# Kernel tuning notes

Hardware: AMD Instinct MI355X
Metric: run time of the kernel (lower is better)

Reference implementation:

```python
import jax, jax.numpy as jnp
import numpy as np

B, N, C = 4, 4096, 128
IK, CK = 9, 9  # inner_k, cross_k
BN_EPS = 1e-5


def setup_inputs() -> dict:
    key = jax.random.key(0)
    ks = jax.random.split(key, 8)
    d = {}
    d["x"] = jax.random.normal(ks[0], (B, N, C), jnp.float32)
    d["y"] = jax.random.normal(ks[1], (B, N, C), jnp.float32)
    d["x_mask"] = jnp.ones((B, N), jnp.float32)
    d["y_mask"] = jnp.ones((B, N), jnp.float32)
    specs = [("mr0", C, 2 * C), ("mr1", C, 2 * C), ("fc", C, C), ("f1", 4 * C, C), ("f2", C, 4 * C)]
    for (name, o, i), k in zip(specs, jax.random.split(ks[2], len(specs))):
        d[name + "_W"] = jax.random.normal(k, (o, i), jnp.float32) * 0.05
        d[name + "_b"] = jnp.zeros((o,), jnp.float32)
        d[name + "_g"] = jnp.ones((o,), jnp.float32)
        d[name + "_beta"] = jnp.zeros((o,), jnp.float32)
        d[name + "_m"] = jnp.zeros((o,), jnp.float32)
        d[name + "_v"] = jnp.ones((o,), jnp.float32)
    return d


def _sqdist(a, b):
    # a: [B,Na,C], b: [B,Nb,C] -> [B,Na,Nb]
    return (jnp.sum(a * a, -1)[:, :, None] + jnp.sum(b * b, -1)[:, None, :]
            - 2.0 * jnp.einsum('bnc,bmc->bnm', a, b))


def _knn(x, y):
    # neighbor indices into concat([x;y]) for every node: [B, Nx+Ny, IK+CK]
    Nx = x.shape[1]
    i_xx = jax.lax.top_k(-_sqdist(x, x), IK)[1]
    i_xy = jax.lax.top_k(-_sqdist(x, y), CK)[1] + Nx
    i_yy = jax.lax.top_k(-_sqdist(y, y), IK)[1] + Nx
    i_yx = jax.lax.top_k(-_sqdist(y, x), CK)[1]
    return jnp.concatenate([jnp.concatenate([i_xx, i_xy], -1),
                            jnp.concatenate([i_yy, i_yx], -1)], axis=1)


def _bn(h, g, b, m, v):
    # eval-mode BatchNorm over channel (last) axis
    return (h - m) * jax.lax.rsqrt(v + BN_EPS) * g + b


def _gelu(h):
    return jax.nn.gelu(h, approximate=False)


def _mrconv(f, nbr, W, b, g, be, m, v):
    # f: [B,Nt,C], nbr: [B,Nt,K] -> Conv(2C->C)+BN+GELU of interleaved [x, max_j(x_j-x_i)]
    xj = jax.vmap(lambda fb, nb: fb[nb])(f, nbr)          # [B,Nt,K,C] gather
    msg = jnp.max(xj - f[:, :, None, :], axis=2)          # [B,Nt,C]
    Bh, Nt, Ch = f.shape
    h = jnp.stack([f, msg], axis=-1).reshape(Bh, Nt, 2 * Ch)  # channel interleave as in torch reshape
    h = jnp.einsum('bnc,oc->bno', h, W) + b
    return _gelu(_bn(h, g, be, m, v))


def _forward(x, x_mask, y, y_mask,
             mr0_W, mr0_b, mr0_g, mr0_beta, mr0_m, mr0_v,
             mr1_W, mr1_b, mr1_g, mr1_beta, mr1_m, mr1_v,
             fc_W, fc_b, fc_g, fc_beta, fc_m, fc_v,
             f1_W, f1_b, f1_g, f1_beta, f1_m, f1_v,
             f2_W, f2_b, f2_g, f2_beta, f2_m, f2_v):
    Nx = x.shape[1]
    nbr = _knn(x, y)
    xy = jnp.concatenate([x, y], axis=1)
    xy = _mrconv(xy, nbr, mr0_W, mr0_b, mr0_g, mr0_beta, mr0_m, mr0_v) + xy
    xy = _mrconv(xy, nbr, mr1_W, mr1_b, mr1_g, mr1_beta, mr1_m, mr1_v) + xy
    xg, yg = xy[:, :Nx], xy[:, Nx:]

    def fc(h):
        return _bn(jnp.einsum('bnc,oc->bno', h, fc_W) + fc_b, fc_g, fc_beta, fc_m, fc_v)

    xo = fc(xg) + x
    yo = fc(yg) + y

    def ffn(h):
        r = h
        h = _gelu(_bn(jnp.einsum('bnc,oc->bno', h, f1_W) + f1_b, f1_g, f1_beta, f1_m, f1_v))
        h = _gelu(_bn(jnp.einsum('bnc,oc->bno', h, f2_W) + f2_b, f2_g, f2_beta, f2_m, f2_v))
        return h + r

    xo = ffn(xo) * x_mask[:, :, None]
    yo = ffn(yo) * y_mask[:, :, None]
    return xo, yo


def reference(x, x_mask, y, y_mask,
              mr0_W, mr0_b, mr0_g, mr0_beta, mr0_m, mr0_v,
              mr1_W, mr1_b, mr1_g, mr1_beta, mr1_m, mr1_v,
              fc_W, fc_b, fc_g, fc_beta, fc_m, fc_v,
              f1_W, f1_b, f1_g, f1_beta, f1_m, f1_v,
              f2_W, f2_b, f2_g, f2_beta, f2_m, f2_v):
    return _forward(x, x_mask, y, y_mask,
                    mr0_W, mr0_b, mr0_g, mr0_beta, mr0_m, mr0_v,
                    mr1_W, mr1_b, mr1_g, mr1_beta, mr1_m, mr1_v,
                    fc_W, fc_b, fc_g, fc_beta, fc_m, fc_v,
                    f1_W, f1_b, f1_g, f1_beta, f1_m, f1_v,
                    f2_W, f2_b, f2_g, f2_beta, f2_m, f2_v)
```

## Files before the change

### kernel.cpp

```cpp
#include <hip/hip_runtime.h>
#include <hip/hip_bf16.h>
#include <float.h>
#include <math.h>

#define BB 4
#define N1 4096
#define NT 8192
#define CH 128
#define NBRS 18
#define ZSEL 2.35f
#define LCAP 40
#define EQ 4096.0f
#define GQGAP 6
#define GQCOV 3

typedef __attribute__((ext_vector_type(8))) short s16x8;
typedef __attribute__((ext_vector_type(16))) float f32x16;

__device__ inline unsigned short f2bf(float v) {
  unsigned u = __float_as_uint(v);
  unsigned r = (u + 0x7FFFu + ((u >> 16) & 1u)) >> 16;
  return (unsigned short)r;
}

__device__ inline unsigned mapf(float f) {
  unsigned u = __float_as_uint(f);
  return (u & 0x80000000u) ? ~u : (u | 0x80000000u);
}

__global__ __launch_bounds__(256) void transpose_k(const float* __restrict__ in,
                                                   float* __restrict__ out,
                                                   int rows, int cols) {
  int t = blockIdx.x * 256 + threadIdx.x;
  if (t < rows * cols) {
    int r = t / cols, c = t % cols;
    out[c * rows + r] = in[t];
  }
}

__global__ __launch_bounds__(256) void norms_concat_k(const float* __restrict__ x,
                                                      const float* __restrict__ y,
                                                      float* __restrict__ xy,
                                                      float* __restrict__ norms) {
  int w = (blockIdx.x * 256 + threadIdx.x) >> 6;
  int lane = threadIdx.x & 63;
  int b = w >> 13, row = w & 8191;
  const float* src = (row < N1) ? (x + ((size_t)b * N1 + row) * CH)
                                : (y + ((size_t)b * N1 + (row - N1)) * CH);
  float2 v = *(const float2*)(src + lane * 2);
  *(float2*)(xy + (size_t)w * CH + lane * 2) = v;
  float s = v.x * v.x + v.y * v.y;
  for (int off = 32; off > 0; off >>= 1) s += __shfl_down(s, off);
  if (lane == 0) norms[w] = s;
}

__global__ __launch_bounds__(256) void cbt_k(const float* __restrict__ xy,
                                             unsigned short* __restrict__ cbt) {
  int t = blockIdx.x * 256 + threadIdx.x;
  int u = t >> 15, p = t & 32767;
  const float* src = xy + (size_t)p * CH + u * 8;
  unsigned hw[4], lw[4];
#pragma unroll
  for (int j = 0; j < 4; ++j) {
    float v0 = src[2 * j], v1 = src[2 * j + 1];
    unsigned short h0 = f2bf(v0), h1 = f2bf(v1);
    float r0 = v0 - __uint_as_float((unsigned)h0 << 16);
    float r1 = v1 - __uint_as_float((unsigned)h1 << 16);
    unsigned short l0 = f2bf(r0), l1 = f2bf(r1);
    hw[j] = (unsigned)h0 | ((unsigned)h1 << 16);
    lw[j] = (unsigned)l0 | ((unsigned)l1 << 16);
  }
  *(uint4*)&cbt[((size_t)u * 32768 + p) * 8] = make_uint4(hw[0], hw[1], hw[2], hw[3]);
  *(uint4*)&cbt[((size_t)(u + 16) * 32768 + p) * 8] = make_uint4(lw[0], lw[1], lw[2], lw[3]);
}

__global__ __launch_bounds__(256) void knn4_k(const unsigned short* __restrict__ cbt,
                                              const float* __restrict__ norms,
                                              int* __restrict__ nbr,
                                              int* __restrict__ cntg,
                                              unsigned* __restrict__ listA,
                                              unsigned* __restrict__ listB,
                                              unsigned short* __restrict__ fbl) {
  __shared__ unsigned short __align__(16) cst[2][32][32][8];
  __shared__ float cn_s[2][32];
  __shared__ unsigned lst[128][2][LCAP];
  __shared__ unsigned short lcnt[128][2];
  const int tid = threadIdx.x;
  const int qblk = blockIdx.x, z = blockIdx.y;
  const int b = z >> 2, combo = z & 3;
  const int qoff = (combo <= 1) ? 0 : N1;
  const int coff = (combo == 0 || combo == 3) ? 0 : N1;
  const int w = tid >> 6;
  const int cl = tid & 31;
  const int h = (tid >> 5) & 1;
  const int h4 = 4 * h;
  const int ql = w * 32 + cl;
  const int q = qblk * 128 + ql;
  const size_t qp = (size_t)b * NT + qoff + q;
  const size_t cb0 = (size_t)b * NT + coff;

  const s16x8* cv = (const s16x8*)cbt;
  s16x8 bh[8], bl[8];
#pragma unroll
  for (int s = 0; s < 8; ++s) {
    bh[s] = cv[(size_t)(2 * s + h) * 32768 + qp];
    bl[s] = cv[(size_t)(16 + 2 * s + h) * 32768 + qp];
  }

  const float nq = norms[qp];
  const float Tc = 128.f - ZSEL * sqrtf(256.f + 4.f * nq);
  int cnt = 0;

  const int su = tid >> 5, sc = tid & 31;
  const char* p0 = (const char*)&cbt[((size_t)(su) * 32768 + cb0 + sc) * 8];
  const char* p1 = (const char*)&cbt[((size_t)(8 + su) * 32768 + cb0 + sc) * 8];
  const char* p2 = (const char*)&cbt[((size_t)(16 + su) * 32768 + cb0 + sc) * 8];
  const char* p3 = (const char*)&cbt[((size_t)(24 + su) * 32768 + cb0 + sc) * 8];
  const float* pn = norms + cb0 + tid;

  uint4 st[4]; float cnreg = 0.f;
  st[0] = *(const uint4*)p0; p0 += 512;
  st[1] = *(const uint4*)p1; p1 += 512;
  st[2] = *(const uint4*)p2; p2 += 512;
  st[3] = *(const uint4*)p3; p3 += 512;
  if (tid < 32) { cnreg = *pn; pn += 32; }
  *(uint4*)&cst[0][su][sc][0] = st[0];
  *(uint4*)&cst[0][8 + su][sc][0] = st[1];
  *(uint4*)&cst[0][16 + su][sc][0] = st[2];
  *(uint4*)&cst[0][24 + su][sc][0] = st[3];
  if (tid < 32) cn_s[0][tid] = cnreg;
  __syncthreads();

  int buf = 0;
  for (int t = 0; t < 128; ++t) {
    if (t < 127) {
      st[0] = *(const uint4*)p0; p0 += 512;
      st[1] = *(const uint4*)p1; p1 += 512;
      st[2] = *(const uint4*)p2; p2 += 512;
      st[3] = *(const uint4*)p3; p3 += 512;
      if (tid < 32) { cnreg = *pn; pn += 32; }
    }
    f32x16 acc = {0.f,0.f,0.f,0.f,0.f,0.f,0.f,0.f,0.f,0.f,0.f,0.f,0.f,0.f,0.f,0.f};
#pragma unroll
    for (int s = 0; s < 8; ++s) {
      s16x8 a0 = *(const s16x8*)&cst[buf][2 * s + h][cl][0];
      s16x8 a1 = *(const s16x8*)&cst[buf][16 + 2 * s + h][cl][0];
      acc = __builtin_amdgcn_mfma_f32_32x32x16_bf16(a0, bh[s], acc, 0, 0, 0);
      acc = __builtin_amdgcn_mfma_f32_32x32x16_bf16(a0, bl[s], acc, 0, 0, 0);
      acc = __builtin_amdgcn_mfma_f32_32x32x16_bf16(a1, bh[s], acc, 0, 0, 0);
    }
    float4 c0 = *(const float4*)&cn_s[buf][h4];
    float4 c1 = *(const float4*)&cn_s[buf][8 + h4];
    float4 c2 = *(const float4*)&cn_s[buf][16 + h4];
    float4 c3 = *(const float4*)&cn_s[buf][24 + h4];
    const float cw[16] = {c0.x, c0.y, c0.z, c0.w, c1.x, c1.y, c1.z, c1.w,
                          c2.x, c2.y, c2.z, c2.w, c3.x, c3.y, c3.z, c3.w};
    const int ib = t * 32 + h4;
#pragma unroll
    for (int g = 0; g < 4; ++g) {
#pragma unroll
      for (int rr = 0; rr < 4; ++rr) {
        const int r = g * 4 + rr;
        float s = fmaf(-2.0f, acc[r], cw[r]);
        if (s <= Tc) {
          int e = (int)((Tc - s) * EQ);
          e = e > 0xFFFFF ? 0xFFFFF : e;
          unsigned key = ((unsigned)e << 12) | (unsigned)(4095 - (ib + g * 8 + rr));
          if (cnt < LCAP) lst[ql][h][cnt] = key;
          ++cnt;
        }
      }
    }
    if (t < 127) {
      *(uint4*)&cst[buf ^ 1][su][sc][0] = st[0];
      *(uint4*)&cst[buf ^ 1][8 + su][sc][0] = st[1];
      *(uint4*)&cst[buf ^ 1][16 + su][sc][0] = st[2];
      *(uint4*)&cst[buf ^ 1][24 + su][sc][0] = st[3];
      if (tid < 32) cn_s[buf ^ 1][tid] = cnreg;
    }
    __syncthreads();
    buf ^= 1;
  }
  lcnt[ql][h] = (unsigned short)cnt;
  __syncthreads();

  if (tid < 128) {
    const int mq = tid;
    const int gq = z * 4096 + qblk * 128 + mq;
    const int c0 = lcnt[mq][0], c1 = lcnt[mq][1];
    const bool over = (c0 > LCAP) || (c1 > LCAP);
    const int n0 = c0 > LCAP ? LCAP : c0;
    const int n1 = c1 > LCAP ? LCAP : c1;
    const int m = n0 + n1;
    unsigned top[10];
#pragma unroll
    for (int j = 0; j < 10; ++j) top[j] = 0u;
    for (int li = 0; li < 2; ++li) {
      const int n = li ? n1 : n0;
      for (int i = 0; i < n; ++i) {
        unsigned key = lst[mq][li][i];
        if (key > top[9]) {
#pragma unroll
          for (int j = 0; j < 10; ++j) {
            bool sw = key > top[j];
            unsigned tv = top[j];
            top[j] = sw ? key : tv;
            key = sw ? tv : key;
          }
        }
      }
    }
    const unsigned e8 = top[8] >> 12, e9 = top[9] >> 12;
    const bool cov = !over && (m >= 9) && (e8 >= GQCOV);
    const bool ok = cov && (m == 9 || (e8 - e9) >= GQGAP);
    const int qg = qblk * 128 + mq;
    const int row = (combo <= 1) ? qg : (N1 + qg);
    const int slot = (combo == 0 || combo == 2) ? 0 : 9;
    const int ioff = (combo == 1 || combo == 2) ? N1 : 0;
    int* dst = nbr + ((size_t)b * NT + row) * NBRS + slot;
    if (ok) {
#pragma unroll
      for (int s = 0; s < 9; ++s)
        dst[s] = (int)(4095u - (top[s] & 0xFFFu)) + ioff;
    } else if (!cov || m > 64) {
      int idx = atomicAdd(&cntg[1], 1);
      listB[idx] = (unsigned)gq;
    } else {
      int idx = atomicAdd(&cntg[0], 1);
      listA[idx] = ((unsigned)m << 16) | (unsigned)gq;
      unsigned short* fp = fbl + (size_t)gq * 64;
      int p = 0;
      for (int i = 0; i < n0; ++i) fp[p++] = (unsigned short)(4095u - (lst[mq][0][i] & 0xFFFu));
      for (int i = 0; i < n1; ++i) fp[p++] = (unsigned short)(4095u - (lst[mq][1][i] & 0xFFFu));
    }
  }
}

__global__ __launch_bounds__(256) void rerank_sl_k(const float* __restrict__ xy,
                                                   const float* __restrict__ norms,
                                                   const unsigned short* __restrict__ fbl,
                                                   const unsigned* __restrict__ listA,
                                                   const int* __restrict__ cntg,
                                                   int* __restrict__ nbr) {
  const int lane = threadIdx.x & 63;
  const int wv = threadIdx.x >> 6;
  const int nA = cntg[0];
  for (int i = blockIdx.x * 4 + wv; i < nA; i += gridDim.x * 4) {
    const unsigned ent = listA[i];
    const int gq = (int)(ent & 0xffffu);
    const int m = (int)(ent >> 16);
    const int z = gq >> 12, q = gq & 4095;
    const int b = z >> 2, combo = z & 3;
    const int qoff = (combo <= 1) ? 0 : N1;
    const int coff = (combo == 0 || combo == 3) ? 0 : N1;
    const size_t cq = (size_t)b * NT + coff;
    const int row = (combo <= 1) ? q : (N1 + q);
    const int slot = (combo == 0 || combo == 2) ? 0 : 9;
    const int ioff = (combo == 1 || combo == 2) ? N1 : 0;
    int* dst = nbr + ((size_t)b * NT + row) * NBRS + slot;
    const float* qrow = xy + ((size_t)b * NT + qoff + q) * CH;

    int ci = 0; float de = FLT_MAX;
    if (lane < m) {
      ci = (int)fbl[(size_t)gq * 64 + lane];
      const float* crow = xy + (cq + ci) * CH;
      const float cnv = norms[cq + ci];
      float a0 = 0.f, a1 = 0.f, a2 = 0.f, a3 = 0.f;
#pragma unroll
      for (int k = 0; k < 32; ++k) {
        float4 qv = *(const float4*)(qrow + k * 4);
        float4 cv2 = *(const float4*)(crow + k * 4);
        a0 = fmaf(qv.x, cv2.x, a0); a1 = fmaf(qv.y, cv2.y, a1);
        a2 = fmaf(qv.z, cv2.z, a2); a3 = fmaf(qv.w, cv2.w, a3);
      }
      de = cnv - 2.0f * ((a0 + a1) + (a2 + a3));
    }
    unsigned long long key = ((unsigned long long)mapf(de) << 32) | (unsigned)ci;
    if (lane >= m) key = ~0ull;
    int xr = 0;
#pragma unroll 1
    for (int k = 0; k < m; ++k) {
      unsigned long long kk = __shfl(key, k);
      xr += (kk < key) ? 1 : 0;
    }
    if (lane < m && xr < 9) dst[xr] = ci + ioff;
  }
}

__global__ __launch_bounds__(256) void rerank_fs_k(const float* __restrict__ xy,
                                                   const float* __restrict__ norms,
                                                   const unsigned* __restrict__ listB,
                                                   const int* __restrict__ cntg,
                                                   int* __restrict__ nbr) {
  __shared__ unsigned long long ms[4][576];
  __shared__ unsigned long long wk[36];
  const int tid = threadIdx.x;
  const int lane = tid & 63, wv = tid >> 6;
  const int nB = cntg[1];
  for (int i = blockIdx.x; i < nB; i += gridDim.x) {
    const int gq = (int)listB[i];
    const int z = gq >> 12, q = gq & 4095;
    const int b = z >> 2, combo = z & 3;
    const int qoff = (combo <= 1) ? 0 : N1;
    const int coff = (combo == 0 || combo == 3) ? 0 : N1;
    const size_t cq = (size_t)b * NT + coff;
    const int row = (combo <= 1) ? q : (N1 + q);
    const int slot = (combo == 0 || combo == 2) ? 0 : 9;
    const int ioff = (combo == 1 || combo == 2) ? N1 : 0;
    int* dst = nbr + ((size_t)b * NT + row) * NBRS + slot;
    const float* qrow = xy + ((size_t)b * NT + qoff + q) * CH;

    unsigned long long bl9[9];
#pragma unroll
    for (int j = 0; j < 9; ++j) bl9[j] = ~0ull;
    for (int it = 0; it < 16; ++it) {
      const int cc = (it * 4 + wv) * 64 + lane;
      const float* crow = xy + (cq + cc) * CH;
      float a0 = 0.f, a1 = 0.f, a2 = 0.f, a3 = 0.f;
#pragma unroll
      for (int k = 0; k < 32; ++k) {
        float4 qv = *(const float4*)(qrow + k * 4);
        float4 cv2 = *(const float4*)(crow + k * 4);
        a0 = fmaf(qv.x, cv2.x, a0); a1 = fmaf(qv.y, cv2.y, a1);
        a2 = fmaf(qv.z, cv2.z, a2); a3 = fmaf(qv.w, cv2.w, a3);
      }
      float d2v = norms[cq + cc] - 2.0f * ((a0 + a1) + (a2 + a3));
      unsigned long long key = ((unsigned long long)mapf(d2v) << 32) | (unsigned)cc;
      if (key < bl9[8]) {
#pragma unroll
        for (int jj = 0; jj < 9; ++jj) {
          bool sw = key < bl9[jj];
          unsigned long long tv = bl9[jj];
          bl9[jj] = sw ? key : tv;
          key = sw ? tv : key;
        }
      }
    }
#pragma unroll
    for (int s = 0; s < 9; ++s) ms[wv][lane * 9 + s] = bl9[s];
    int ptr = 0;
    for (int s = 0; s < 9; ++s) {
      unsigned long long hd = ms[wv][lane * 9 + ptr];
      unsigned long long mn = hd;
#pragma unroll
      for (int off = 1; off < 64; off <<= 1) {
        unsigned long long ot = __shfl_xor(mn, off);
        mn = (ot < mn) ? ot : mn;
      }
      unsigned long long wm = __ballot(hd == mn);
      int wl = __ffsll(wm) - 1;
      if (lane == wl) ptr++;
      if (lane == 0) wk[wv * 9 + s] = mn;
    }
    __syncthreads();
    if (wv == 0) {
      unsigned long long key = (lane < 36) ? wk[lane] : ~0ull;
      int xr = 0;
#pragma unroll 1
      for (int k = 0; k < 36; ++k) {
        unsigned long long kk = __shfl(key, k);
        xr += (kk < key) ? 1 : 0;
      }
      if (lane < 36 && xr < 9) dst[xr] = (int)(unsigned)(key & 0xffffffffull) + ioff;
    }
    __syncthreads();
  }
}

__global__ __launch_bounds__(256) void mrconv_k(const float* __restrict__ in,
                                                const int* __restrict__ nbr,
                                                const float* __restrict__ Wt,
                                                const float* __restrict__ bias,
                                                const float* __restrict__ gam,
                                                const float* __restrict__ bet,
                                                const float* __restrict__ mean,
                                                const float* __restrict__ var,
                                                float* __restrict__ out) {
  __shared__ float h[32][260];
  const int tid = threadIdx.x;
  const int pt0 = blockIdx.x * 32;
  {
    const int w = tid >> 6, lane = tid & 63;
    for (int pp = 0; pp < 8; ++pp) {
      const int p = w * 8 + pp;
      const int n = pt0 + p;
      const int b = n >> 13;
      const float* frow = in + (size_t)n * CH;
      float2 f2 = *(const float2*)(frow + lane * 2);
      float mx = -FLT_MAX, my = -FLT_MAX;
      const int* nb = nbr + (size_t)n * NBRS;
      for (int j = 0; j < NBRS; ++j) {
        int idx = nb[j];
        const float* vrow = in + ((size_t)b * NT + idx) * CH;
        float2 v2 = *(const float2*)(vrow + lane * 2);
        mx = fmaxf(mx, v2.x - f2.x);
        my = fmaxf(my, v2.y - f2.y);
      }
      h[p][lane * 4 + 0] = f2.x; h[p][lane * 4 + 1] = mx;
      h[p][lane * 4 + 2] = f2.y; h[p][lane * 4 + 3] = my;
    }
  }
  __syncthreads();
  const int o = tid & 127, gg = tid >> 7;
  float acc[16];
#pragma unroll
  for (int p = 0; p < 16; ++p) acc[p] = 0.f;
  for (int k = 0; k < 256; k += 4) {
    float w0 = Wt[(k + 0) * CH + o], w1 = Wt[(k + 1) * CH + o];
    float w2 = Wt[(k + 2) * CH + o], w3 = Wt[(k + 3) * CH + o];
#pragma unroll
    for (int p = 0; p < 16; ++p) {
      float4 hv = *(const float4*)&h[gg * 16 + p][k];
      acc[p] = fmaf(hv.x, w0, acc[p]);
      acc[p] = fmaf(hv.y, w1, acc[p]);
      acc[p] = fmaf(hv.z, w2, acc[p]);
      acc[p] = fmaf(hv.w, w3, acc[p]);
    }
  }
  const float sc = gam[o] / sqrtf(var[o] + 1e-5f);
  const float bs = bias[o], mo = mean[o], be = bet[o];
#pragma unroll
  for (int p = 0; p < 16; ++p) {
    const int n = pt0 + gg * 16 + p;
    float hv = acc[p] + bs;
    float bn = (hv - mo) * sc + be;
    float gl = 0.5f * bn * (1.0f + erff(bn * 0.70710678118654752f));
    out[(size_t)n * CH + o] = gl + h[gg * 16 + p][2 * o];
  }
}

__global__ __launch_bounds__(256) void fc_k(const float* __restrict__ in,
                                            const float* __restrict__ Wt,
                                            const float* __restrict__ bias,
                                            const float* __restrict__ gam,
                                            const float* __restrict__ bet,
                                            const float* __restrict__ mean,
                                            const float* __restrict__ var,
                                            const float* __restrict__ xres,
                                            const float* __restrict__ yres,
                                            float* __restrict__ out) {
  __shared__ float s[32][132];
  const int tid = threadIdx.x;
  const int pt0 = blockIdx.x * 32;
  {
    const int w = tid >> 6, lane = tid & 63;
    for (int pp = 0; pp < 8; ++pp) {
      const int p = w * 8 + pp, n = pt0 + p;
      float2 v = *(const float2*)(in + (size_t)n * CH + lane * 2);
      s[p][lane * 2] = v.x; s[p][lane * 2 + 1] = v.y;
    }
  }
  __syncthreads();
  const int o = tid & 127, gg = tid >> 7;
  float acc[16];
#pragma unroll
  for (int p = 0; p < 16; ++p) acc[p] = 0.f;
  for (int k = 0; k < 128; k += 4) {
    float w0 = Wt[(k + 0) * CH + o], w1 = Wt[(k + 1) * CH + o];
    float w2 = Wt[(k + 2) * CH + o], w3 = Wt[(k + 3) * CH + o];
#pragma unroll
    for (int p = 0; p < 16; ++p) {
      float4 hv = *(const float4*)&s[gg * 16 + p][k];
      acc[p] = fmaf(hv.x, w0, fmaf(hv.y, w1, fmaf(hv.z, w2, fmaf(hv.w, w3, acc[p]))));
    }
  }
  const float sc = gam[o] / sqrtf(var[o] + 1e-5f);
  const float bs = bias[o], mo = mean[o], be = bet[o];
#pragma unroll
  for (int p = 0; p < 16; ++p) {
    const int n = pt0 + gg * 16 + p;
    const int b = n >> 13, row = n & 8191;
    float bn = (acc[p] + bs - mo) * sc + be;
    float res = (row < N1) ? xres[((size_t)b * N1 + row) * CH + o]
                           : yres[((size_t)b * N1 + row - N1) * CH + o];
    out[(size_t)n * CH + o] = bn + res;
  }
}

__global__ __launch_bounds__(256) void ffn_k(const float* __restrict__ u,
                                             const float* __restrict__ W1t,
                                             const float* __restrict__ b1,
                                             const float* __restrict__ g1,
                                             const float* __restrict__ be1,
                                             const float* __restrict__ m1,
                                             const float* __restrict__ v1,
                                             const float* __restrict__ W2t,
                                             const float* __restrict__ b2,
                                             const float* __restrict__ g2,
                                             const float* __restrict__ be2,
                                             const float* __restrict__ m2,
                                             const float* __restrict__ v2,
                                             const float* __restrict__ xmask,
                                             const float* __restrict__ ymask,
                                             float* __restrict__ outbuf) {
  __shared__ float su[16][132];
  __shared__ float h1[16][516];
  const int tid = threadIdx.x;
  const int pt0 = blockIdx.x * 16;
  {
    const int w = tid >> 6, lane = tid & 63;
    for (int pp = 0; pp < 4; ++pp) {
      const int p = w * 4 + pp, n = pt0 + p;
      float2 v = *(const float2*)(u + (size_t)n * CH + lane * 2);
      su[p][lane * 2] = v.x; su[p][lane * 2 + 1] = v.y;
    }
  }
  __syncthreads();
  {
    const int o2 = tid;
    float a1[16], a2[16];
#pragma unroll
    for (int p = 0; p < 16; ++p) { a1[p] = 0.f; a2[p] = 0.f; }
    for (int k = 0; k < 128; k += 2) {
      float wA0 = W1t[(k + 0) * 512 + o2], wB0 = W1t[(k + 0) * 512 + o2 + 256];
      float wA1 = W1t[(k + 1) * 512 + o2], wB1 = W1t[(k + 1) * 512 + o2 + 256];
#pragma unroll
      for (int p = 0; p < 16; ++p) {
        float2 uv = *(const float2*)&su[p][k];
        a1[p] = fmaf(uv.x, wA0, fmaf(uv.y, wA1, a1[p]));
        a2[p] = fmaf(uv.x, wB0, fmaf(uv.y, wB1, a2[p]));
      }
    }
    float scA = g1[o2] / sqrtf(v1[o2] + 1e-5f);
    float scB = g1[o2 + 256] / sqrtf(v1[o2 + 256] + 1e-5f);
    float bsA = b1[o2], moA = m1[o2], beA = be1[o2];
    float bsB = b1[o2 + 256], moB = m1[o2 + 256], beB = be1[o2 + 256];
#pragma unroll
    for (int p = 0; p < 16; ++p) {
      float hA = (a1[p] + bsA - moA) * scA + beA;
      float hB = (a2[p] + bsB - moB) * scB + beB;
      h1[p][o2] = 0.5f * hA * (1.0f + erff(hA * 0.70710678118654752f));
      h1[p][o2 + 256] = 0.5f * hB * (1.0f + erff(hB * 0.70710678118654752f));
    }
  }
  __syncthreads();
  const int o = tid & 127, gg = tid >> 7;
  float acc[8];
#pragma unroll
  for (int p = 0; p < 8; ++p) acc[p] = 0.f;
  for (int k = 0; k < 512; k += 4) {
    float w0 = W2t[(k + 0) * CH + o], w1 = W2t[(k + 1) * CH + o];
    float w2 = W2t[(k + 2) * CH + o], w3 = W2t[(k + 3) * CH + o];
#pragma unroll
    for (int p = 0; p < 8; ++p) {
      float4 hv = *(const float4*)&h1[gg * 8 + p][k];
      acc[p] = fmaf(hv.x, w0, fmaf(hv.y, w1, fmaf(hv.z, w2, fmaf(hv.w, w3, acc[p]))));
    }
  }
  const float sc = g2[o] / sqrtf(v2[o] + 1e-5f);
  const float bs = b2[o], mo = m2[o], be = be2[o];
#pragma unroll
  for (int p = 0; p < 8; ++p) {
    const int n = pt0 + gg * 8 + p;
    const int b = n >> 13, row = n & 8191;
    float bn = (acc[p] + bs - mo) * sc + be;
    float gl = 0.5f * bn * (1.0f + erff(bn * 0.70710678118654752f));
    float res = su[gg * 8 + p][o];
    float msk; size_t oidx;
    if (row < N1) {
      msk = xmask[(size_t)b * N1 + row];
      oidx = ((size_t)b * N1 + row) * CH + o;
    } else {
      msk = ymask[(size_t)b * N1 + row - N1];
      oidx = (size_t)BB * N1 * CH + ((size_t)b * N1 + row - N1) * CH + o;
    }
    outbuf[oidx] = (gl + res) * msk;
  }
}

extern "C" void kernel_launch(void* const* d_in, const int* in_sizes, int n_in,
                              void* d_out, int out_size, void* d_ws, size_t ws_size,
                              hipStream_t stream) {
  const float* x  = (const float*)d_in[0];
  const float* y  = (const float*)d_in[1];
  const float* xm = (const float*)d_in[2];
  const float* ym = (const float*)d_in[3];
  const float* mr0W = (const float*)d_in[4];
  const float* mr1W = (const float*)d_in[10];
  const float* fcW  = (const float*)d_in[16];
  const float* f1W  = (const float*)d_in[22];
  const float* f2W  = (const float*)d_in[28];

  char* ws = (char*)d_ws;
  float*          xyA   = (float*)(ws + 0);
  unsigned short* cbt   = (unsigned short*)(ws + 16777216);
  float*          xyB   = (float*)(ws + 16777216);
  float*          norms = (float*)(ws + 33554432);
  int*            cntg  = (int*)(ws + 33685504);
  unsigned*       listA = (unsigned*)(ws + 33689600);
  unsigned*       listB = (unsigned*)(ws + 33951744);
  unsigned short* fbl   = (unsigned short*)(ws + 34213888);
  int*            nbr   = (int*)(ws + 42602496);
  float*          mr0t  = (float*)(ws + 44961792);
  float*          mr1t  = (float*)(ws + 45092864);
  float*          fct   = (float*)(ws + 45223936);
  float*          f1t   = (float*)(ws + 45289472);
  float*          f2t   = (float*)(ws + 45551616);

  hipMemsetAsync(cntg, 0, 8, stream);

  transpose_k<<<(128 * 256 + 255) / 256, 256, 0, stream>>>(mr0W, mr0t, 128, 256);
  transpose_k<<<(128 * 256 + 255) / 256, 256, 0, stream>>>(mr1W, mr1t, 128, 256);
  transpose_k<<<(128 * 128 + 255) / 256, 256, 0, stream>>>(fcW, fct, 128, 128);
  transpose_k<<<(512 * 128 + 255) / 256, 256, 0, stream>>>(f1W, f1t, 512, 128);
  transpose_k<<<(128 * 512 + 255) / 256, 256, 0, stream>>>(f2W, f2t, 128, 512);

  norms_concat_k<<<8192, 256, 0, stream>>>(x, y, xyA, norms);
  cbt_k<<<2048, 256, 0, stream>>>(xyA, cbt);
  knn4_k<<<dim3(32, 16), 256, 0, stream>>>(cbt, norms, nbr, cntg, listA, listB, fbl);
  rerank_sl_k<<<256, 256, 0, stream>>>(xyA, norms, fbl, listA, cntg, nbr);
  rerank_fs_k<<<256, 256, 0, stream>>>(xyA, norms, listB, cntg, nbr);

  mrconv_k<<<1024, 256, 0, stream>>>(xyA, nbr, mr0t,
      (const float*)d_in[5], (const float*)d_in[6], (const float*)d_in[7],
      (const float*)d_in[8], (const float*)d_in[9], xyB);
  mrconv_k<<<1024, 256, 0, stream>>>(xyB, nbr, mr1t,
      (const float*)d_in[11], (const float*)d_in[12], (const float*)d_in[13],
      (const float*)d_in[14], (const float*)d_in[15], xyA);

  fc_k<<<1024, 256, 0, stream>>>(xyA, fct,
      (const float*)d_in[17], (const float*)d_in[18], (const float*)d_in[19],
      (const float*)d_in[20], (const float*)d_in[21], x, y, xyB);

  ffn_k<<<2048, 256, 0, stream>>>(xyB,
      f1t, (const float*)d_in[23], (const float*)d_in[24], (const float*)d_in[25],
      (const float*)d_in[26], (const float*)d_in[27],
      f2t, (const float*)d_in[29], (const float*)d_in[30], (const float*)d_in[31],
      (const float*)d_in[32], (const float*)d_in[33],
      xm, ym, (float*)d_out);
}
```

Baseline: 670.2 us.

## Keep per-thread top-12 candidates in registers and double queries per KNN block

The KNN kernel now keeps a register-resident sorted top-12 list per thread instead of appending threshold-passing candidates into a large shared-memory list. Blocks grow to 512 threads covering 256 queries, so each staged candidate tile is reused by twice as many queries and fewer tile loads are issued per thread. The final selection becomes a two-way merge of the sorted per-half lists, and the fallback candidate buffer shrinks from 64 to 24 entries. The overflow check is dropped, so queries with more than 12 candidates per half now go through the approximate path instead of full search, which may change accuracy. The unrolled insertion sort also adds register pressure.

```diff
diff --git a/kernel.cpp b/kernel.cpp
--- a/kernel.cpp
+++ b/kernel.cpp
@@ -9,10 +9,10 @@
 #define CH 128
 #define NBRS 18
 #define ZSEL 2.35f
-#define LCAP 40
 #define EQ 4096.0f
 #define GQGAP 6
 #define GQCOV 3
+#define QPB 256
 
 typedef __attribute__((ext_vector_type(8))) short s16x8;
 typedef __attribute__((ext_vector_type(16))) float f32x16;
@@ -27,6 +27,18 @@
   unsigned u = __float_as_uint(f);
   return (u & 0x80000000u) ? ~u : (u | 0x80000000u);
 }
+
+#define INS12U(l, key0)                         \
+  {                                             \
+    unsigned nk = key0;                         \
+    _Pragma("unroll")                           \
+    for (int j = 0; j < 12; ++j) {              \
+      bool sw = nk > l[j];                      \
+      unsigned tv = l[j];                       \
+      l[j] = sw ? nk : tv;                      \
+      nk = sw ? tv : nk;                        \
+    }                                           \
+  }
 
 __global__ __launch_bounds__(256) void transpose_k(const float* __restrict__ in,
                                                    float* __restrict__ out,
@@ -74,17 +86,16 @@
   *(uint4*)&cbt[((size_t)(u + 16) * 32768 + p) * 8] = make_uint4(lw[0], lw[1], lw[2], lw[3]);
 }
 
-__global__ __launch_bounds__(256) void knn4_k(const unsigned short* __restrict__ cbt,
-                                              const float* __restrict__ norms,
-                                              int* __restrict__ nbr,
-                                              int* __restrict__ cntg,
-                                              unsigned* __restrict__ listA,
-                                              unsigned* __restrict__ listB,
-                                              unsigned short* __restrict__ fbl) {
+__global__ __launch_bounds__(512, 2) void knn8_k(const unsigned short* __restrict__ cbt,
+                                                 const float* __restrict__ norms,
+                                                 int* __restrict__ nbr,
+                                                 int* __restrict__ cntg,
+                                                 unsigned* __restrict__ listA,
+                                                 unsigned* __restrict__ listB,
+                                                 unsigned short* __restrict__ fbl) {
   __shared__ unsigned short __align__(16) cst[2][32][32][8];
   __shared__ float cn_s[2][32];
-  __shared__ unsigned lst[128][2][LCAP];
-  __shared__ unsigned short lcnt[128][2];
+  __shared__ unsigned short cnt2[QPB][2];
   const int tid = threadIdx.x;
   const int qblk = blockIdx.x, z = blockIdx.y;
   const int b = z >> 2, combo = z & 3;
@@ -95,7 +106,7 @@
   const int h = (tid >> 5) & 1;
   const int h4 = 4 * h;
   const int ql = w * 32 + cl;
-  const int q = qblk * 128 + ql;
+  const int q = qblk * QPB + ql;
   const size_t qp = (size_t)b * NT + qoff + q;
   const size_t cb0 = (size_t)b * NT + coff;
 
@@ -110,34 +121,30 @@
   const float nq = norms[qp];
   const float Tc = 128.f - ZSEL * sqrtf(256.f + 4.f * nq);
   int cnt = 0;
-
-  const int su = tid >> 5, sc = tid & 31;
+  unsigned lA[12];
+#pragma unroll
+  for (int j = 0; j < 12; ++j) lA[j] = 0u;
+
+  const int su = tid >> 5;
+  const int sc = tid & 31;
   const char* p0 = (const char*)&cbt[((size_t)(su) * 32768 + cb0 + sc) * 8];
-  const char* p1 = (const char*)&cbt[((size_t)(8 + su) * 32768 + cb0 + sc) * 8];
-  const char* p2 = (const char*)&cbt[((size_t)(16 + su) * 32768 + cb0 + sc) * 8];
-  const char* p3 = (const char*)&cbt[((size_t)(24 + su) * 32768 + cb0 + sc) * 8];
+  const char* p1 = (const char*)&cbt[((size_t)(16 + su) * 32768 + cb0 + sc) * 8];
   const float* pn = norms + cb0 + tid;
 
-  uint4 st[4]; float cnreg = 0.f;
-  st[0] = *(const uint4*)p0; p0 += 512;
-  st[1] = *(const uint4*)p1; p1 += 512;
-  st[2] = *(const uint4*)p2; p2 += 512;
-  st[3] = *(const uint4*)p3; p3 += 512;
+  uint4 st0, st1; float cnreg = 0.f;
+  st0 = *(const uint4*)p0; p0 += 512;
+  st1 = *(const uint4*)p1; p1 += 512;
   if (tid < 32) { cnreg = *pn; pn += 32; }
-  *(uint4*)&cst[0][su][sc][0] = st[0];
-  *(uint4*)&cst[0][8 + su][sc][0] = st[1];
-  *(uint4*)&cst[0][16 + su][sc][0] = st[2];
-  *(uint4*)&cst[0][24 + su][sc][0] = st[3];
+  *(uint4*)&cst[0][su][sc][0] = st0;
+  *(uint4*)&cst[0][16 + su][sc][0] = st1;
   if (tid < 32) cn_s[0][tid] = cnreg;
   __syncthreads();
 
   int buf = 0;
   for (int t = 0; t < 128; ++t) {
     if (t < 127) {
-      st[0] = *(const uint4*)p0; p0 += 512;
-      st[1] = *(const uint4*)p1; p1 += 512;
-      st[2] = *(const uint4*)p2; p2 += 512;
-      st[3] = *(const uint4*)p3; p3 += 512;
+      st0 = *(const uint4*)p0; p0 += 512;
+      st1 = *(const uint4*)p1; p1 += 512;
       if (tid < 32) { cnreg = *pn; pn += 32; }
     }
     f32x16 acc = {0.f,0.f,0.f,0.f,0.f,0.f,0.f,0.f,0.f,0.f,0.f,0.f,0.f,0.f,0.f,0.f};
@@ -157,63 +164,54 @@
                           c2.x, c2.y, c2.z, c2.w, c3.x, c3.y, c3.z, c3.w};
     const int ib = t * 32 + h4;
 #pragma unroll
-    for (int g = 0; g < 4; ++g) {
-#pragma unroll
-      for (int rr = 0; rr < 4; ++rr) {
-        const int r = g * 4 + rr;
-        float s = fmaf(-2.0f, acc[r], cw[r]);
-        if (s <= Tc) {
-          int e = (int)((Tc - s) * EQ);
-          e = e > 0xFFFFF ? 0xFFFFF : e;
-          unsigned key = ((unsigned)e << 12) | (unsigned)(4095 - (ib + g * 8 + rr));
-          if (cnt < LCAP) lst[ql][h][cnt] = key;
-          ++cnt;
-        }
+    for (int r = 0; r < 16; ++r) {
+      const int idx = ib + (r & 3) + 8 * (r >> 2);
+      float s = fmaf(-2.0f, acc[r], cw[r]);
+      if (s <= Tc) {
+        ++cnt;
+        int e = (int)((Tc - s) * EQ);
+        e = e > 0xFFFFF ? 0xFFFFF : e;
+        unsigned key = ((unsigned)e << 12) | (unsigned)(4095 - idx);
+        if (key > lA[11]) INS12U(lA, key);
       }
     }
     if (t < 127) {
-      *(uint4*)&cst[buf ^ 1][su][sc][0] = st[0];
-      *(uint4*)&cst[buf ^ 1][8 + su][sc][0] = st[1];
-      *(uint4*)&cst[buf ^ 1][16 + su][sc][0] = st[2];
-      *(uint4*)&cst[buf ^ 1][24 + su][sc][0] = st[3];
+      *(uint4*)&cst[buf ^ 1][su][sc][0] = st0;
+      *(uint4*)&cst[buf ^ 1][16 + su][sc][0] = st1;
       if (tid < 32) cn_s[buf ^ 1][tid] = cnreg;
     }
     __syncthreads();
     buf ^= 1;
   }
-  lcnt[ql][h] = (unsigned short)cnt;
+
+  unsigned* dmp = (unsigned*)&cst[0][0][0][0];
+#pragma unroll
+  for (int j = 0; j < 12; ++j) dmp[((size_t)ql * 2 + h) * 12 + j] = lA[j];
+  cnt2[ql][h] = (unsigned short)(cnt > 65535 ? 65535 : cnt);
   __syncthreads();
 
-  if (tid < 128) {
+  if (tid < QPB) {
     const int mq = tid;
-    const int gq = z * 4096 + qblk * 128 + mq;
-    const int c0 = lcnt[mq][0], c1 = lcnt[mq][1];
-    const bool over = (c0 > LCAP) || (c1 > LCAP);
-    const int n0 = c0 > LCAP ? LCAP : c0;
-    const int n1 = c1 > LCAP ? LCAP : c1;
-    const int m = n0 + n1;
-    unsigned top[10];
-#pragma unroll
-    for (int j = 0; j < 10; ++j) top[j] = 0u;
-    for (int li = 0; li < 2; ++li) {
-      const int n = li ? n1 : n0;
-      for (int i = 0; i < n; ++i) {
-        unsigned key = lst[mq][li][i];
-        if (key > top[9]) {
-#pragma unroll
-          for (int j = 0; j < 10; ++j) {
-            bool sw = key > top[j];
-            unsigned tv = top[j];
-            top[j] = sw ? key : tv;
-            key = sw ? tv : key;
-          }
-        }
-      }
-    }
-    const unsigned e8 = top[8] >> 12, e9 = top[9] >> 12;
-    const bool cov = !over && (m >= 9) && (e8 >= GQCOV);
-    const bool ok = cov && (m == 9 || (e8 - e9) >= GQGAP);
-    const int qg = qblk * 128 + mq;
+    const int qg = qblk * QPB + mq;
+    const int gq = z * 4096 + qg;
+    const int c0 = cnt2[mq][0], c1 = cnt2[mq][1];
+    const int k0 = c0 > 12 ? 12 : c0, k1 = c1 > 12 ? 12 : c1;
+    const int m_true = c0 + c1;
+    const unsigned* pa = &dmp[((size_t)mq * 2 + 0) * 12];
+    const unsigned* pb = &dmp[((size_t)mq * 2 + 1) * 12];
+    unsigned mg[10];
+    int i = 0, j = 0;
+#pragma unroll
+    for (int s = 0; s < 10; ++s) {
+      unsigned av = (i < k0) ? pa[i] : 0u;
+      unsigned bv = (j < k1) ? pb[j] : 0u;
+      bool ta = av >= bv;
+      mg[s] = ta ? av : bv;
+      if (ta) ++i; else ++j;
+    }
+    const unsigned e8 = mg[8] >> 12, e9 = mg[9] >> 12;
+    const bool cov = (m_true >= 9) && (e8 >= GQCOV);
+    const bool ok = cov && (m_true == 9 || (e8 - e9) >= GQGAP);
     const int row = (combo <= 1) ? qg : (N1 + qg);
     const int slot = (combo == 0 || combo == 2) ? 0 : 9;
     const int ioff = (combo == 1 || combo == 2) ? N1 : 0;
@@ -221,17 +219,17 @@
     if (ok) {
 #pragma unroll
       for (int s = 0; s < 9; ++s)
-        dst[s] = (int)(4095u - (top[s] & 0xFFFu)) + ioff;
-    } else if (!cov || m > 64) {
+        dst[s] = (int)(4095u - (mg[s] & 0xFFFu)) + ioff;
+    } else if (!cov) {
       int idx = atomicAdd(&cntg[1], 1);
       listB[idx] = (unsigned)gq;
     } else {
       int idx = atomicAdd(&cntg[0], 1);
-      listA[idx] = ((unsigned)m << 16) | (unsigned)gq;
-      unsigned short* fp = fbl + (size_t)gq * 64;
+      listA[idx] = ((unsigned)(k0 + k1) << 16) | (unsigned)gq;
+      unsigned short* fp = fbl + (size_t)gq * 24;
       int p = 0;
-      for (int i = 0; i < n0; ++i) fp[p++] = (unsigned short)(4095u - (lst[mq][0][i] & 0xFFFu));
-      for (int i = 0; i < n1; ++i) fp[p++] = (unsigned short)(4095u - (lst[mq][1][i] & 0xFFFu));
+      for (int t2 = 0; t2 < k0; ++t2) fp[p++] = (unsigned short)(4095u - (pa[t2] & 0xFFFu));
+      for (int t2 = 0; t2 < k1; ++t2) fp[p++] = (unsigned short)(4095u - (pb[t2] & 0xFFFu));
     }
   }
 }
@@ -262,7 +260,7 @@
 
     int ci = 0; float de = FLT_MAX;
     if (lane < m) {
-      ci = (int)fbl[(size_t)gq * 64 + lane];
+      ci = (int)fbl[(size_t)gq * 24 + lane];
       const float* crow = xy + (cq + ci) * CH;
       const float cnv = norms[cq + ci];
       float a0 = 0.f, a1 = 0.f, a2 = 0.f, a3 = 0.f;
@@ -590,12 +588,12 @@
   unsigned*       listA = (unsigned*)(ws + 33689600);
   unsigned*       listB = (unsigned*)(ws + 33951744);
   unsigned short* fbl   = (unsigned short*)(ws + 34213888);
-  int*            nbr   = (int*)(ws + 42602496);
-  float*          mr0t  = (float*)(ws + 44961792);
-  float*          mr1t  = (float*)(ws + 45092864);
-  float*          fct   = (float*)(ws + 45223936);
-  float*          f1t   = (float*)(ws + 45289472);
-  float*          f2t   = (float*)(ws + 45551616);
+  int*            nbr   = (int*)(ws + 37748736);
+  float*          mr0t  = (float*)(ws + 40108032);
+  float*          mr1t  = (float*)(ws + 40239104);
+  float*          fct   = (float*)(ws + 40370176);
+  float*          f1t   = (float*)(ws + 40435712);
+  float*          f2t   = (float*)(ws + 40697856);
 
   hipMemsetAsync(cntg, 0, 8, stream);
 
@@ -607,7 +605,7 @@
 
   norms_concat_k<<<8192, 256, 0, stream>>>(x, y, xyA, norms);
   cbt_k<<<2048, 256, 0, stream>>>(xyA, cbt);
-  knn4_k<<<dim3(32, 16), 256, 0, stream>>>(cbt, norms, nbr, cntg, listA, listB, fbl);
+  knn8_k<<<dim3(16, 16), 512, 0, stream>>>(cbt, norms, nbr, cntg, listA, listB, fbl);
   rerank_sl_k<<<256, 256, 0, stream>>>(xyA, norms, fbl, listA, cntg, nbr);
   rerank_fs_k<<<256, 256, 0, stream>>>(xyA, norms, listB, cntg, nbr);
 
```

After: 713.3 us. 1.06x slower.

## Move fc and FFN projections onto bf16x3 MFMA with split-precision operands

Applied to the files above, without the earlier changes.

Replaces the scalar fp32 FMA matmuls in the fc and FFN kernels with 16x16x32 bf16 MFMA instructions. Each operand is split into hi and lo bf16 parts and three products are summed to keep near-fp32 accuracy. Weights are pre-split by a new kernel instead of being transposed, and activations are split into LDS tiles of 16 rows. The FFN hidden layer is also stored split in LDS. The aim is to cut the ALU cost of these dense layers, at the price of extra conversion work, uncached global weight reads per wave, and a small loss of precision.

```diff
diff --git a/kernel.cpp b/kernel.cpp
--- a/kernel.cpp
+++ b/kernel.cpp
@@ -16,16 +16,22 @@
 
 typedef __attribute__((ext_vector_type(8))) short s16x8;
 typedef __attribute__((ext_vector_type(16))) float f32x16;
+typedef __attribute__((ext_vector_type(4))) float f32x4;
 
 __device__ inline unsigned short f2bf(float v) {
   unsigned u = __float_as_uint(v);
   unsigned r = (u + 0x7FFFu + ((u >> 16) & 1u)) >> 16;
   return (unsigned short)r;
 }
-
+__device__ inline float bf2f(unsigned short h) {
+  return __uint_as_float((unsigned)h << 16);
+}
 __device__ inline unsigned mapf(float f) {
   unsigned u = __float_as_uint(f);
   return (u & 0x80000000u) ? ~u : (u | 0x80000000u);
+}
+__device__ inline float gelu_f(float x) {
+  return 0.5f * x * (1.0f + erff(x * 0.70710678118654752f));
 }
 
 __global__ __launch_bounds__(256) void transpose_k(const float* __restrict__ in,
@@ -35,6 +41,19 @@
   if (t < rows * cols) {
     int r = t / cols, c = t % cols;
     out[c * rows + r] = in[t];
+  }
+}
+
+__global__ __launch_bounds__(256) void wsplit_k(const float* __restrict__ w,
+                                                unsigned short* __restrict__ hi,
+                                                unsigned short* __restrict__ lo,
+                                                int n) {
+  int t = blockIdx.x * 256 + threadIdx.x;
+  if (t < n) {
+    float v = w[t];
+    unsigned short h = f2bf(v);
+    float r = v - bf2f(h);
+    hi[t] = h; lo[t] = f2bf(r);
   }
 }
 
@@ -64,8 +83,8 @@
   for (int j = 0; j < 4; ++j) {
     float v0 = src[2 * j], v1 = src[2 * j + 1];
     unsigned short h0 = f2bf(v0), h1 = f2bf(v1);
-    float r0 = v0 - __uint_as_float((unsigned)h0 << 16);
-    float r1 = v1 - __uint_as_float((unsigned)h1 << 16);
+    float r0 = v0 - bf2f(h0);
+    float r1 = v1 - bf2f(h1);
     unsigned short l0 = f2bf(r0), l1 = f2bf(r1);
     hw[j] = (unsigned)h0 | ((unsigned)h1 << 16);
     lw[j] = (unsigned)l0 | ((unsigned)l1 << 16);
@@ -429,142 +448,191 @@
   }
 }
 
-__global__ __launch_bounds__(256) void fc_k(const float* __restrict__ in,
-                                            const float* __restrict__ Wt,
-                                            const float* __restrict__ bias,
-                                            const float* __restrict__ gam,
-                                            const float* __restrict__ bet,
-                                            const float* __restrict__ mean,
-                                            const float* __restrict__ var,
-                                            const float* __restrict__ xres,
-                                            const float* __restrict__ yres,
-                                            float* __restrict__ out) {
-  __shared__ float s[32][132];
-  const int tid = threadIdx.x;
-  const int pt0 = blockIdx.x * 32;
-  {
-    const int w = tid >> 6, lane = tid & 63;
-    for (int pp = 0; pp < 8; ++pp) {
-      const int p = w * 8 + pp, n = pt0 + p;
-      float2 v = *(const float2*)(in + (size_t)n * CH + lane * 2);
-      s[p][lane * 2] = v.x; s[p][lane * 2 + 1] = v.y;
-    }
-  }
-  __syncthreads();
-  const int o = tid & 127, gg = tid >> 7;
-  float acc[16];
-#pragma unroll
-  for (int p = 0; p < 16; ++p) acc[p] = 0.f;
-  for (int k = 0; k < 128; k += 4) {
-    float w0 = Wt[(k + 0) * CH + o], w1 = Wt[(k + 1) * CH + o];
-    float w2 = Wt[(k + 2) * CH + o], w3 = Wt[(k + 3) * CH + o];
-#pragma unroll
-    for (int p = 0; p < 16; ++p) {
-      float4 hv = *(const float4*)&s[gg * 16 + p][k];
-      acc[p] = fmaf(hv.x, w0, fmaf(hv.y, w1, fmaf(hv.z, w2, fmaf(hv.w, w3, acc[p]))));
-    }
-  }
-  const float sc = gam[o] / sqrtf(var[o] + 1e-5f);
-  const float bs = bias[o], mo = mean[o], be = bet[o];
-#pragma unroll
-  for (int p = 0; p < 16; ++p) {
-    const int n = pt0 + gg * 16 + p;
-    const int b = n >> 13, row = n & 8191;
-    float bn = (acc[p] + bs - mo) * sc + be;
-    float res = (row < N1) ? xres[((size_t)b * N1 + row) * CH + o]
-                           : yres[((size_t)b * N1 + row - N1) * CH + o];
-    out[(size_t)n * CH + o] = bn + res;
-  }
-}
-
-__global__ __launch_bounds__(256) void ffn_k(const float* __restrict__ u,
-                                             const float* __restrict__ W1t,
-                                             const float* __restrict__ b1,
-                                             const float* __restrict__ g1,
-                                             const float* __restrict__ be1,
-                                             const float* __restrict__ m1,
-                                             const float* __restrict__ v1,
-                                             const float* __restrict__ W2t,
-                                             const float* __restrict__ b2,
-                                             const float* __restrict__ g2,
-                                             const float* __restrict__ be2,
-                                             const float* __restrict__ m2,
-                                             const float* __restrict__ v2,
-                                             const float* __restrict__ xmask,
-                                             const float* __restrict__ ymask,
-                                             float* __restrict__ outbuf) {
-  __shared__ float su[16][132];
-  __shared__ float h1[16][516];
+__global__ __launch_bounds__(256) void fc2_k(const float* __restrict__ in,
+                                             const unsigned short* __restrict__ Whi,
+                                             const unsigned short* __restrict__ Wlo,
+                                             const float* __restrict__ bias,
+                                             const float* __restrict__ gam,
+                                             const float* __restrict__ bet,
+                                             const float* __restrict__ mean,
+                                             const float* __restrict__ var,
+                                             const float* __restrict__ xres,
+                                             const float* __restrict__ yres,
+                                             float* __restrict__ out) {
+  __shared__ unsigned short __align__(16) aHi[16][16][8];
+  __shared__ unsigned short __align__(16) aLo[16][16][8];
   const int tid = threadIdx.x;
   const int pt0 = blockIdx.x * 16;
   {
-    const int w = tid >> 6, lane = tid & 63;
-    for (int pp = 0; pp < 4; ++pp) {
-      const int p = w * 4 + pp, n = pt0 + p;
-      float2 v = *(const float2*)(u + (size_t)n * CH + lane * 2);
-      su[p][lane * 2] = v.x; su[p][lane * 2 + 1] = v.y;
+    const int row = tid >> 4, ku = tid & 15;
+    const float* src = in + (size_t)(pt0 + row) * CH + ku * 8;
+    unsigned hw[4], lw[4];
+#pragma unroll
+    for (int j = 0; j < 4; ++j) {
+      float v0 = src[2 * j], v1 = src[2 * j + 1];
+      unsigned short h0 = f2bf(v0), h1 = f2bf(v1);
+      float r0 = v0 - bf2f(h0), r1 = v1 - bf2f(h1);
+      hw[j] = (unsigned)h0 | ((unsigned)f2bf(v1) << 16);
+      hw[j] = (unsigned)h0 | ((unsigned)h1 << 16);
+      lw[j] = (unsigned)f2bf(r0) | ((unsigned)f2bf(r1) << 16);
+    }
+    *(uint4*)&aHi[ku][row][0] = make_uint4(hw[0], hw[1], hw[2], hw[3]);
+    *(uint4*)&aLo[ku][row][0] = make_uint4(lw[0], lw[1], lw[2], lw[3]);
+  }
+  __syncthreads();
+  const int lane = tid & 63, w = tid >> 6;
+  const int r16 = lane & 15, kg = lane >> 4;
+  f32x4 acc[2] = {{0.f,0.f,0.f,0.f}, {0.f,0.f,0.f,0.f}};
+#pragma unroll
+  for (int ks = 0; ks < 4; ++ks) {
+    s16x8 ah = *(const s16x8*)&aHi[ks * 4 + kg][r16][0];
+    s16x8 al = *(const s16x8*)&aLo[ks * 4 + kg][r16][0];
+#pragma unroll
+    for (int cb = 0; cb < 2; ++cb) {
+      const int o = w * 32 + cb * 16 + r16;
+      s16x8 bh2 = *(const s16x8*)(Whi + o * 128 + ks * 32 + kg * 8);
+      s16x8 bl2 = *(const s16x8*)(Wlo + o * 128 + ks * 32 + kg * 8);
+      acc[cb] = __builtin_amdgcn_mfma_f32_16x16x32_bf16(ah, bh2, acc[cb], 0, 0, 0);
+      acc[cb] = __builtin_amdgcn_mfma_f32_16x16x32_bf16(ah, bl2, acc[cb], 0, 0, 0);
+      acc[cb] = __builtin_amdgcn_mfma_f32_16x16x32_bf16(al, bh2, acc[cb], 0, 0, 0);
+    }
+  }
+#pragma unroll
+  for (int cb = 0; cb < 2; ++cb) {
+    const int o = w * 32 + cb * 16 + r16;
+    const float sc = gam[o] / sqrtf(var[o] + 1e-5f);
+    const float bs = bias[o], mo = mean[o], be = bet[o];
+#pragma unroll
+    for (int rg = 0; rg < 4; ++rg) {
+      const int row = kg * 4 + rg;
+      const int n = pt0 + row;
+      const int b = n >> 13, prow = n & 8191;
+      float bn = (acc[cb][rg] + bs - mo) * sc + be;
+      float res = (prow < N1) ? xres[((size_t)b * N1 + prow) * CH + o]
+                              : yres[((size_t)b * N1 + prow - N1) * CH + o];
+      out[(size_t)n * CH + o] = bn + res;
+    }
+  }
+}
+
+__global__ __launch_bounds__(256) void ffn2_k(const float* __restrict__ u,
+                                              const unsigned short* __restrict__ W1hi,
+                                              const unsigned short* __restrict__ W1lo,
+                                              const float* __restrict__ b1,
+                                              const float* __restrict__ g1,
+                                              const float* __restrict__ be1,
+                                              const float* __restrict__ m1,
+                                              const float* __restrict__ v1,
+                                              const unsigned short* __restrict__ W2hi,
+                                              const unsigned short* __restrict__ W2lo,
+                                              const float* __restrict__ b2,
+                                              const float* __restrict__ g2,
+                                              const float* __restrict__ be2,
+                                              const float* __restrict__ m2,
+                                              const float* __restrict__ v2,
+                                              const float* __restrict__ xmask,
+                                              const float* __restrict__ ymask,
+                                              float* __restrict__ outbuf) {
+  __shared__ unsigned short __align__(16) aHi[16][16][8];
+  __shared__ unsigned short __align__(16) aLo[16][16][8];
+  __shared__ unsigned short __align__(16) hHi[64][16][8];
+  __shared__ unsigned short __align__(16) hLo[64][16][8];
+  const int tid = threadIdx.x;
+  const int pt0 = blockIdx.x * 16;
+  {
+    const int row = tid >> 4, ku = tid & 15;
+    const float* src = u + (size_t)(pt0 + row) * CH + ku * 8;
+    unsigned hw[4], lw[4];
+#pragma unroll
+    for (int j = 0; j < 4; ++j) {
+      float v0 = src[2 * j], v1 = src[2 * j + 1];
+      unsigned short h0 = f2bf(v0), h1 = f2bf(v1);
+      float r0 = v0 - bf2f(h0), r1 = v1 - bf2f(h1);
+      hw[j] = (unsigned)h0 | ((unsigned)h1 << 16);
+      lw[j] = (unsigned)f2bf(r0) | ((unsigned)f2bf(r1) << 16);
+    }
+    *(uint4*)&aHi[ku][row][0] = make_uint4(hw[0], hw[1], hw[2], hw[3]);
+    *(uint4*)&aLo[ku][row][0] = make_uint4(lw[0], lw[1], lw[2], lw[3]);
+  }
+  __syncthreads();
+  const int lane = tid & 63, w = tid >> 6;
+  const int r16 = lane & 15, kg = lane >> 4;
+  {
+    f32x4 acc[8];
+#pragma unroll
+    for (int cb = 0; cb < 8; ++cb) acc[cb] = {0.f, 0.f, 0.f, 0.f};
+#pragma unroll
+    for (int ks = 0; ks < 4; ++ks) {
+      s16x8 ah = *(const s16x8*)&aHi[ks * 4 + kg][r16][0];
+      s16x8 al = *(const s16x8*)&aLo[ks * 4 + kg][r16][0];
+#pragma unroll
+      for (int cb = 0; cb < 8; ++cb) {
+        const int o = w * 128 + cb * 16 + r16;
+        s16x8 bh2 = *(const s16x8*)(W1hi + o * 128 + ks * 32 + kg * 8);
+        s16x8 bl2 = *(const s16x8*)(W1lo + o * 128 + ks * 32 + kg * 8);
+        acc[cb] = __builtin_amdgcn_mfma_f32_16x16x32_bf16(ah, bh2, acc[cb], 0, 0, 0);
+        acc[cb] = __builtin_amdgcn_mfma_f32_16x16x32_bf16(ah, bl2, acc[cb], 0, 0, 0);
+        acc[cb] = __builtin_amdgcn_mfma_f32_16x16x32_bf16(al, bh2, acc[cb], 0, 0, 0);
+      }
+    }
+#pragma unroll
+    for (int cb = 0; cb < 8; ++cb) {
+      const int o = w * 128 + cb * 16 + r16;
+      const float sc = g1[o] / sqrtf(v1[o] + 1e-5f);
+      const float bs = b1[o], mo = m1[o], be = be1[o];
+#pragma unroll
+      for (int rg = 0; rg < 4; ++rg) {
+        const int row = kg * 4 + rg;
+        float bn = (acc[cb][rg] + bs - mo) * sc + be;
+        float gl = gelu_f(bn);
+        unsigned short hb = f2bf(gl);
+        float rr = gl - bf2f(hb);
+        hHi[o >> 3][row][o & 7] = hb;
+        hLo[o >> 3][row][o & 7] = f2bf(rr);
+      }
     }
   }
   __syncthreads();
   {
-    const int o2 = tid;
-    float a1[16], a2[16];
-#pragma unroll
-    for (int p = 0; p < 16; ++p) { a1[p] = 0.f; a2[p] = 0.f; }
-    for (int k = 0; k < 128; k += 2) {
-      float wA0 = W1t[(k + 0) * 512 + o2], wB0 = W1t[(k + 0) * 512 + o2 + 256];
-      float wA1 = W1t[(k + 1) * 512 + o2], wB1 = W1t[(k + 1) * 512 + o2 + 256];
-#pragma unroll
-      for (int p = 0; p < 16; ++p) {
-        float2 uv = *(const float2*)&su[p][k];
-        a1[p] = fmaf(uv.x, wA0, fmaf(uv.y, wA1, a1[p]));
-        a2[p] = fmaf(uv.x, wB0, fmaf(uv.y, wB1, a2[p]));
-      }
-    }
-    float scA = g1[o2] / sqrtf(v1[o2] + 1e-5f);
-    float scB = g1[o2 + 256] / sqrtf(v1[o2 + 256] + 1e-5f);
-    float bsA = b1[o2], moA = m1[o2], beA = be1[o2];
-    float bsB = b1[o2 + 256], moB = m1[o2 + 256], beB = be1[o2 + 256];
-#pragma unroll
-    for (int p = 0; p < 16; ++p) {
-      float hA = (a1[p] + bsA - moA) * scA + beA;
-      float hB = (a2[p] + bsB - moB) * scB + beB;
-      h1[p][o2] = 0.5f * hA * (1.0f + erff(hA * 0.70710678118654752f));
-      h1[p][o2 + 256] = 0.5f * hB * (1.0f + erff(hB * 0.70710678118654752f));
-    }
-  }
-  __syncthreads();
-  const int o = tid & 127, gg = tid >> 7;
-  float acc[8];
-#pragma unroll
-  for (int p = 0; p < 8; ++p) acc[p] = 0.f;
-  for (int k = 0; k < 512; k += 4) {
-    float w0 = W2t[(k + 0) * CH + o], w1 = W2t[(k + 1) * CH + o];
-    float w2 = W2t[(k + 2) * CH + o], w3 = W2t[(k + 3) * CH + o];
-#pragma unroll
-    for (int p = 0; p < 8; ++p) {
-      float4 hv = *(const float4*)&h1[gg * 8 + p][k];
-      acc[p] = fmaf(hv.x, w0, fmaf(hv.y, w1, fmaf(hv.z, w2, fmaf(hv.w, w3, acc[p]))));
-    }
-  }
-  const float sc = g2[o] / sqrtf(v2[o] + 1e-5f);
-  const float bs = b2[o], mo = m2[o], be = be2[o];
-#pragma unroll
-  for (int p = 0; p < 8; ++p) {
-    const int n = pt0 + gg * 8 + p;
-    const int b = n >> 13, row = n & 8191;
-    float bn = (acc[p] + bs - mo) * sc + be;
-    float gl = 0.5f * bn * (1.0f + erff(bn * 0.70710678118654752f));
-    float res = su[gg * 8 + p][o];
-    float msk; size_t oidx;
-    if (row < N1) {
-      msk = xmask[(size_t)b * N1 + row];
-      oidx = ((size_t)b * N1 + row) * CH + o;
-    } else {
-      msk = ymask[(size_t)b * N1 + row - N1];
-      oidx = (size_t)BB * N1 * CH + ((size_t)b * N1 + row - N1) * CH + o;
-    }
-    outbuf[oidx] = (gl + res) * msk;
+    f32x4 acc[2] = {{0.f,0.f,0.f,0.f}, {0.f,0.f,0.f,0.f}};
+#pragma unroll
+    for (int ks = 0; ks < 16; ++ks) {
+      s16x8 ah = *(const s16x8*)&hHi[ks * 4 + kg][r16][0];
+      s16x8 al = *(const s16x8*)&hLo[ks * 4 + kg][r16][0];
+#pragma unroll
+      for (int cb = 0; cb < 2; ++cb) {
+        const int o = w * 32 + cb * 16 + r16;
+        s16x8 bh2 = *(const s16x8*)(W2hi + o * 512 + ks * 32 + kg * 8);
+        s16x8 bl2 = *(const s16x8*)(W2lo + o * 512 + ks * 32 + kg * 8);
+        acc[cb] = __builtin_amdgcn_mfma_f32_16x16x32_bf16(ah, bh2, acc[cb], 0, 0, 0);
+        acc[cb] = __builtin_amdgcn_mfma_f32_16x16x32_bf16(ah, bl2, acc[cb], 0, 0, 0);
+        acc[cb] = __builtin_amdgcn_mfma_f32_16x16x32_bf16(al, bh2, acc[cb], 0, 0, 0);
+      }
+    }
+#pragma unroll
+    for (int cb = 0; cb < 2; ++cb) {
+      const int o = w * 32 + cb * 16 + r16;
+      const float sc = g2[o] / sqrtf(v2[o] + 1e-5f);
+      const float bs = b2[o], mo = m2[o], be = be2[o];
+#pragma unroll
+      for (int rg = 0; rg < 4; ++rg) {
+        const int row = kg * 4 + rg;
+        const int n = pt0 + row;
+        const int b = n >> 13, prow = n & 8191;
+        float bn = (acc[cb][rg] + bs - mo) * sc + be;
+        float gl = gelu_f(bn);
+        float res = u[(size_t)n * CH + o];
+        float msk; size_t oidx;
+        if (prow < N1) {
+          msk = xmask[(size_t)b * N1 + prow];
+          oidx = ((size_t)b * N1 + prow) * CH + o;
+        } else {
+          msk = ymask[(size_t)b * N1 + prow - N1];
+          oidx = (size_t)BB * N1 * CH + ((size_t)b * N1 + prow - N1) * CH + o;
+        }
+        outbuf[oidx] = (gl + res) * msk;
+      }
+    }
   }
 }
 
@@ -593,17 +661,20 @@
   int*            nbr   = (int*)(ws + 42602496);
   float*          mr0t  = (float*)(ws + 44961792);
   float*          mr1t  = (float*)(ws + 45092864);
-  float*          fct   = (float*)(ws + 45223936);
-  float*          f1t   = (float*)(ws + 45289472);
-  float*          f2t   = (float*)(ws + 45551616);
+  unsigned short* fcWhi = (unsigned short*)(ws + 45223936);
+  unsigned short* fcWlo = (unsigned short*)(ws + 45256704);
+  unsigned short* f1hi  = (unsigned short*)(ws + 45289472);
+  unsigned short* f1lo  = (unsigned short*)(ws + 45420544);
+  unsigned short* f2hi  = (unsigned short*)(ws + 45551616);
+  unsigned short* f2lo  = (unsigned short*)(ws + 45682688);
 
   hipMemsetAsync(cntg, 0, 8, stream);
 
   transpose_k<<<(128 * 256 + 255) / 256, 256, 0, stream>>>(mr0W, mr0t, 128, 256);
   transpose_k<<<(128 * 256 + 255) / 256, 256, 0, stream>>>(mr1W, mr1t, 128, 256);
-  transpose_k<<<(128 * 128 + 255) / 256, 256, 0, stream>>>(fcW, fct, 128, 128);
-  transpose_k<<<(512 * 128 + 255) / 256, 256, 0, stream>>>(f1W, f1t, 512, 128);
-  transpose_k<<<(128 * 512 + 255) / 256, 256, 0, stream>>>(f2W, f2t, 128, 512);
+  wsplit_k<<<64, 256, 0, stream>>>(fcW, fcWhi, fcWlo, 128 * 128);
+  wsplit_k<<<256, 256, 0, stream>>>(f1W, f1hi, f1lo, 512 * 128);
+  wsplit_k<<<256, 256, 0, stream>>>(f2W, f2hi, f2lo, 128 * 512);
 
   norms_concat_k<<<8192, 256, 0, stream>>>(x, y, xyA, norms);
   cbt_k<<<2048, 256, 0, stream>>>(xyA, cbt);
@@ -618,14 +689,14 @@
       (const float*)d_in[11], (const float*)d_in[12], (const float*)d_in[13],
       (const float*)d_in[14], (const float*)d_in[15], xyA);
 
-  fc_k<<<1024, 256, 0, stream>>>(xyA, fct,
+  fc2_k<<<2048, 256, 0, stream>>>(xyA, fcWhi, fcWlo,
       (const float*)d_in[17], (const float*)d_in[18], (const float*)d_in[19],
       (const float*)d_in[20], (const float*)d_in[21], x, y, xyB);
 
-  ffn_k<<<2048, 256, 0, stream>>>(xyB,
-      f1t, (const float*)d_in[23], (const float*)d_in[24], (const float*)d_in[25],
+  ffn2_k<<<2048, 256, 0, stream>>>(xyB,
+      f1hi, f1lo, (const float*)d_in[23], (const float*)d_in[24], (const float*)d_in[25],
       (const float*)d_in[26], (const float*)d_in[27],
-      f2t, (const float*)d_in[29], (const float*)d_in[30], (const float*)d_in[31],
+      f2hi, f2lo, (const float*)d_in[29], (const float*)d_in[30], (const float*)d_in[31],
       (const float*)d_in[32], (const float*)d_in[33],
       xm, ym, (float*)d_out);
 }
```

New measurement: 623.0 us. 7.0% less time.
